# Performance work log

Measured on AMD Instinct MI355X. Metric: run time of the kernel, lower is better.

## Reference

```python
import jax, jax.numpy as jnp
import numpy as np

ALPHA = 1.702
LIMIT = 7.0


def setup_inputs() -> dict:
    key = jax.random.key(0)
    ks = jax.random.split(key, 6)
    T, H, D, E = 8192, 1024, 1024, 8
    hidden_states = jax.random.normal(ks[0], (T, H), dtype=jnp.float32)
    routing_weights = jax.random.uniform(ks[1], (T, E), dtype=jnp.float32)
    # 0.02 scale keeps activations in a sane range (original uses raw randn params)
    gate_up_proj = jax.random.normal(ks[2], (E, H, 2 * D), dtype=jnp.float32) * 0.02
    gate_up_proj_bias = jax.random.normal(ks[3], (E, 2 * D), dtype=jnp.float32) * 0.02
    down_proj = jax.random.normal(ks[4], (E, D, H), dtype=jnp.float32) * 0.02
    down_proj_bias = jax.random.normal(ks[5], (E, H), dtype=jnp.float32) * 0.02
    return {
        "hidden_states": hidden_states,
        "routing_weights": routing_weights,
        "gate_up_proj": gate_up_proj,
        "gate_up_proj_bias": gate_up_proj_bias,
        "down_proj": down_proj,
        "down_proj_bias": down_proj_bias,
    }


def reference(hidden_states, routing_weights, gate_up_proj, gate_up_proj_bias,
              down_proj, down_proj_bias):
    # hidden_states: [T, H]; routing_weights: [T, E] (batch_size == T in the torch code)
    B, H = hidden_states.shape[0], hidden_states.shape[-1]
    hs = hidden_states.reshape(-1, H)  # [T, H]
    # all-experts batched GEMM: [E, T, 2D]
    gate_up = jnp.einsum('th,ehd->etd', hs, gate_up_proj) + gate_up_proj_bias[:, None, :]
    gate = jnp.minimum(gate_up[..., ::2], LIMIT)          # [E, T, D]
    up = jnp.clip(gate_up[..., 1::2], -LIMIT, LIMIT)      # [E, T, D]
    glu = gate * jax.nn.sigmoid(gate * ALPHA)
    # down projection: [E, T, H]
    next_states = jnp.einsum('etd,edh->eth', (up + 1.0) * glu, down_proj) \
        + down_proj_bias[:, None, :]
    # routing-weighted combine over experts: [T, H]
    out = jnp.einsum('eth,te->th', next_states, routing_weights)
    return out.reshape(B, -1, H)  # [T, 1, H], matching final .view(batch_size, -1, hidden)
```

## Files before the change

kernel.cpp:

```cpp
#include <hip/hip_runtime.h>
#include <hip/hip_bf16.h>

#define T_DIM 8192
#define H_DIM 1024
#define D_DIM 1024
#define E_DIM 8
#define TWO_D 2048
#define K2 8192

#define ALPHA_C 1.702f
#define LIMIT_C 7.0f

typedef __attribute__((ext_vector_type(8))) short s8v;
typedef __attribute__((ext_vector_type(4))) float f4v;

__device__ __forceinline__ void g2l16(const void* g, void* l) {
    __builtin_amdgcn_global_load_lds((const __attribute__((address_space(1))) void*)g,
                                     (__attribute__((address_space(3))) void*)l, 16, 0, 0);
}

__device__ __forceinline__ unsigned short f2bf(float f) {
    __hip_bfloat16 h = __float2bfloat16(f);
    return __builtin_bit_cast(unsigned short, h);
}

#define FEN asm volatile("" ::: "memory")
#define BARR { FEN; __builtin_amdgcn_s_barrier(); FEN; }
#define VMW0 asm volatile("s_waitcnt vmcnt(0)" ::: "memory")


__global__ void f32_to_bf16_kernel(const float* __restrict__ in,
                                   unsigned short* __restrict__ out, size_t n) {
    size_t i = ((size_t)blockIdx.x * blockDim.x + threadIdx.x) * 4;
    if (i + 3 < n) {
        float4 v = *(const float4*)(in + i);
        ushort4 o;
        o.x = f2bf(v.x); o.y = f2bf(v.y); o.z = f2bf(v.z); o.w = f2bf(v.w);
        *(ushort4*)(out + i) = o;
    }
}

__global__ void transpose_conv_kernel(const float* __restrict__ in,
                                      unsigned short* __restrict__ out,
                                      int cols, size_t ibs, size_t obs, size_t ors,
                                      int remap) {
    __shared__ float t[32][33];
    const int b = blockIdx.z;
    const int c0 = blockIdx.x * 32, r0 = blockIdx.y * 32;
    const int tx = threadIdx.x & 31, ty = threadIdx.x >> 5;
    const float* ip = in + (size_t)b * ibs;
    #pragma unroll
    for (int i = 0; i < 4; ++i)
        t[ty + i * 8][tx] = ip[(size_t)(r0 + ty + i * 8) * cols + c0 + tx];
    __syncthreads();
    unsigned short* op = out + (size_t)b * obs;
    #pragma unroll
    for (int i = 0; i < 4; ++i) {
        int c = c0 + ty + i * 8;
        int nc = remap ? ((c & ~31) + ((c & 1) << 4) + ((c >> 1) & 15)) : c;
        op[(size_t)nc * ors + r0 + tx] = f2bf(t[tx][ty + i * 8]);
    }
}

__global__ void transpose_w3_tiled_kernel(const float* __restrict__ in,
                                          unsigned short* __restrict__ out) {
    __shared__ float t[32][33];
    const int e = blockIdx.z;
    const int c0 = blockIdx.x * 32;
    const int r0 = blockIdx.y * 32;
    const int tx = threadIdx.x & 31, ty = threadIdx.x >> 5;
    const float* ip = in + (size_t)e * D_DIM * H_DIM;
    #pragma unroll
    for (int i = 0; i < 4; ++i)
        t[ty + i * 8][tx] = ip[(size_t)(r0 + ty + i * 8) * H_DIM + c0 + tx];
    __syncthreads();
    #pragma unroll
    for (int i = 0; i < 4; ++i) {
        const int hcol = c0 + ty + i * 8;
        const int kk = e * D_DIM + r0 + tx;
        const int nt = hcol >> 7, rIn = hcol & 127;
        const int kt = kk >> 6, c = kk & 63;
        out[((size_t)nt * 128 + kt) * 8192 + rIn * 64 + (c ^ ((rIn & 7) << 3))] =
            f2bf(t[tx][ty + i * 8]);
    }
}


__global__ __launch_bounds__(256, 2) void gemm1_kernel(
    const short* __restrict__ Ag0,
    const short* __restrict__ Bg0,
    const float* __restrict__ b1,
    const float* __restrict__ rw,
    unsigned short* __restrict__ act2t)
{
    const int e = blockIdx.z;
    const int mBase = blockIdx.x * 128;
    const int nBase = blockIdx.y * 128;
    const int tid = threadIdx.x;
    const int lane = tid & 63;
    const int wave = tid >> 6;
    const int wm = wave >> 1, wn = wave & 1;
    const int cq = lane & 15, quad = lane >> 4;

    __shared__ __align__(16) short As[128 * 64];
    __shared__ __align__(16) short Bs[128 * 64];

    const short* Ag = Ag0 + (size_t)mBase * H_DIM;
    const short* Bg = Bg0 + ((size_t)e * TWO_D + nBase) * H_DIM;

    f4v acc[4][4];
    #pragma unroll
    for (int mt = 0; mt < 4; ++mt)
        #pragma unroll
        for (int nt = 0; nt < 4; ++nt)
            acc[mt][nt] = (f4v){0.f, 0.f, 0.f, 0.f};

    const int srow8 = lane >> 3;
    const int gco = ((lane & 7) ^ srow8) * 8;
    const int cq7 = cq & 7;

    for (int k0 = 0; k0 < H_DIM; k0 += 64) {
        #pragma unroll
        for (int i = 0; i < 4; ++i) {
            const int r = wave * 32 + i * 8 + srow8;
            g2l16(Ag + (size_t)r * H_DIM + k0 + gco, As + (wave * 32 + i * 8) * 64);
            g2l16(Bg + (size_t)r * H_DIM + k0 + gco, Bs + (wave * 32 + i * 8) * 64);
        }
        __syncthreads();
        #pragma unroll
        for (int h = 0; h < 2; ++h) {
            s8v af[4], bf[4];
            const int pc = (((h << 2) + quad) ^ cq7) * 8;
            #pragma unroll
            for (int i = 0; i < 4; ++i) {
                af[i] = *(const s8v*)(As + (wm * 64 + i * 16 + cq) * 64 + pc);
                bf[i] = *(const s8v*)(Bs + (wn * 64 + i * 16 + cq) * 64 + pc);
            }
            #pragma unroll
            for (int mt = 0; mt < 4; ++mt)
                #pragma unroll
                for (int nt = 0; nt < 4; ++nt)
                    acc[mt][nt] = __builtin_amdgcn_mfma_f32_16x16x32_bf16(
                        af[mt], bf[nt], acc[mt][nt], 0, 0, 0);
        }
        __syncthreads();
    }

    float rwv[4][4];
    #pragma unroll
    for (int mt = 0; mt < 4; ++mt)
        #pragma unroll
        for (int r = 0; r < 4; ++r)
            rwv[mt][r] = rw[(size_t)(mBase + wm * 64 + mt * 16 + quad * 4 + r) * E_DIM + e];

    const int kt_blk = e * 16 + (nBase >> 7);
    unsigned short* tb = act2t + ((size_t)blockIdx.x * 128 + kt_blk) * 8192;

    #pragma unroll
    for (int p = 0; p < 2; ++p) {
        const int j = (((nBase + wn * 64 + p * 32) >> 5) << 4) + cq;
        const float gb = b1[(size_t)e * TWO_D + 2 * j];
        const float ub = b1[(size_t)e * TWO_D + 2 * j + 1];
        const int c = wn * 32 + p * 16 + cq;
        #pragma unroll
        for (int mt = 0; mt < 4; ++mt) {
            #pragma unroll
            for (int r = 0; r < 4; ++r) {
                float gate = acc[mt][2 * p][r] + gb;
                float up   = acc[mt][2 * p + 1][r] + ub;
                gate = fminf(gate, LIMIT_C);
                up = fminf(fmaxf(up, -LIMIT_C), LIMIT_C);
                float glu = gate / (1.f + __expf(-ALPHA_C * gate));
                float a = (up + 1.f) * glu * rwv[mt][r];
                const int rIn = wm * 64 + mt * 16 + quad * 4 + r;
                tb[rIn * 64 + (c ^ ((rIn & 7) << 3))] = f2bf(a);
            }
        }
    }
}


__global__ __launch_bounds__(512, 1) void gemm2_kernel(
    const short* __restrict__ At,
    const short* __restrict__ Bt,
    const float* __restrict__ rw,
    const float* __restrict__ b3,
    float* __restrict__ out)
{
    const int id = blockIdx.x;
    const int mIdx = id & 31;
    const int nIdx = id >> 5;
    const int tid = threadIdx.x;
    const int lane = tid & 63;
    const int wave = tid >> 6;
    const int wm = wave >> 1, wn = wave & 1;
    const int cq = lane & 15, quad = lane >> 4;
    const int cq7 = cq & 7;

    __shared__ __align__(16) short As[2][256 * 64];
    __shared__ __align__(16) short Bs[2][128 * 64];

    f4v acc[4][4];
    #pragma unroll
    for (int mt = 0; mt < 4; ++mt)
        #pragma unroll
        for (int nt = 0; nt < 4; ++nt)
            acc[mt][nt] = (f4v){0.f, 0.f, 0.f, 0.f};

    const int lane8 = lane * 8;

#define G2STAGE(KT, BUF)                                                          \
    { const size_t _kt = (size_t)(KT);                                            \
      _Pragma("unroll")                                                           \
      for (int i = 0; i < 4; ++i) {                                               \
          const int R = wave * 32 + i * 8;                                        \
          const short* _s = At + ((size_t)(2 * mIdx + (R >> 7)) * 128 + _kt) * 8192 \
                          + (R & 127) * 64 + lane8;                               \
          g2l16(_s, &As[BUF][R * 64]);                                            \
      }                                                                           \
      _Pragma("unroll")                                                           \
      for (int i = 0; i < 2; ++i) {                                               \
          const int R = wave * 16 + i * 8;                                        \
          const short* _s = Bt + ((size_t)nIdx * 128 + _kt) * 8192 + R * 64 + lane8; \
          g2l16(_s, &Bs[BUF][R * 64]);                                            \
      } }

    G2STAGE(0, 0);
    VMW0;
    BARR;

    int cur = 0;
    #pragma unroll 1
    for (int kt = 0; kt < 128; ++kt) {
        if (kt + 1 < 128) { G2STAGE(kt + 1, cur ^ 1); }
        FEN;
        const short* Ab = As[cur];
        const short* Bb = Bs[cur];
        __builtin_amdgcn_s_setprio(1);
        #pragma unroll
        for (int h = 0; h < 2; ++h) {
            s8v af[4], bf[4];
            const int pc = (((h << 2) + quad) ^ cq7) * 8;
            #pragma unroll
            for (int i = 0; i < 4; ++i) {
                af[i] = *(const s8v*)(Ab + (wm * 64 + i * 16 + cq) * 64 + pc);
                bf[i] = *(const s8v*)(Bb + (wn * 64 + i * 16 + cq) * 64 + pc);
            }
            #pragma unroll
            for (int mt = 0; mt < 4; ++mt)
                #pragma unroll
                for (int nt = 0; nt < 4; ++nt)
                    acc[mt][nt] = __builtin_amdgcn_mfma_f32_16x16x32_bf16(
                        af[mt], bf[nt], acc[mt][nt], 0, 0, 0);
        }
        __builtin_amdgcn_s_setprio(0);
        VMW0;
        BARR;
        cur ^= 1;
    }

    const int mBase = mIdx * 256;
    const int nBase = nIdx * 128;
    #pragma unroll
    for (int mt = 0; mt < 4; ++mt) {
        #pragma unroll
        for (int r = 0; r < 4; ++r) {
            const int row = mBase + wm * 64 + mt * 16 + quad * 4 + r;
            const float4 rwa = *(const float4*)(rw + (size_t)row * E_DIM);
            const float4 rwb = *(const float4*)(rw + (size_t)row * E_DIM + 4);
            #pragma unroll
            for (int nt = 0; nt < 4; ++nt) {
                const int col = nBase + wn * 64 + nt * 16 + cq;
                float bias = rwa.x * b3[0 * H_DIM + col] + rwa.y * b3[1 * H_DIM + col]
                           + rwa.z * b3[2 * H_DIM + col] + rwa.w * b3[3 * H_DIM + col]
                           + rwb.x * b3[4 * H_DIM + col] + rwb.y * b3[5 * H_DIM + col]
                           + rwb.z * b3[6 * H_DIM + col] + rwb.w * b3[7 * H_DIM + col];
                out[(size_t)row * H_DIM + col] = acc[mt][nt][r] + bias;
            }
        }
    }
}


extern "C" void kernel_launch(void* const* d_in, const int* in_sizes, int n_in,
                              void* d_out, int out_size, void* d_ws, size_t ws_size,
                              hipStream_t stream) {
    const float* hs = (const float*)d_in[0];
    const float* rw = (const float*)d_in[1];
    const float* w1 = (const float*)d_in[2];
    const float* b1 = (const float*)d_in[3];
    const float* w3 = (const float*)d_in[4];
    const float* b3 = (const float*)d_in[5];
    float* out = (float*)d_out;

    char* ws = (char*)d_ws;
    unsigned short* hsb   = (unsigned short*)(ws);
    unsigned short* w1b   = (unsigned short*)(ws + ((size_t)16 << 20));
    unsigned short* w3t   = (unsigned short*)(ws + ((size_t)48 << 20));
    unsigned short* act2t = (unsigned short*)(ws + ((size_t)64 << 20));

    {
        size_t n = (size_t)T_DIM * H_DIM;
        f32_to_bf16_kernel<<<dim3(n / (256 * 4)), dim3(256), 0, stream>>>(hs, hsb, n);
    }
    transpose_conv_kernel<<<dim3(TWO_D / 32, H_DIM / 32, E_DIM), dim3(256), 0, stream>>>(
        w1, w1b, TWO_D, (size_t)H_DIM * TWO_D, (size_t)TWO_D * H_DIM, (size_t)H_DIM, 1);
    transpose_w3_tiled_kernel<<<dim3(H_DIM / 32, D_DIM / 32, E_DIM), dim3(256), 0, stream>>>(
        w3, w3t);
    gemm1_kernel<<<dim3(T_DIM / 128, TWO_D / 128, E_DIM), dim3(256), 0, stream>>>(
        (const short*)hsb, (const short*)w1b, b1, rw, act2t);
    gemm2_kernel<<<dim3(256), dim3(512), 0, stream>>>(
        (const short*)act2t, (const short*)w3t, rw, b3, out);
}
```

Baseline: 614.0 us.

## Split-K gemm2 into two halves, enlarge gemm1 tiles, move bias to reduce kernel

gemm2 now splits the 8192-long K dimension into two halves across 512 blocks of 256 threads, with each block computing a 256x128 tile. It drops the double-buffered LDS pipeline in favour of single-buffered loads. One half writes to out and the other to a workspace partial, and a new reduce kernel sums them and adds the routing-weighted down bias. gemm1's M tile doubles to 256 rows per block to reuse B fragments more. This is meant to raise occupancy and parallelism in gemm2, at the cost of an extra full-size fp32 read/write pass. The partial buffer reuses the hsb workspace region, which is safe only because gemm1 has already consumed hsb.

```diff
diff --git a/kernel.cpp b/kernel.cpp
--- a/kernel.cpp
+++ b/kernel.cpp
@@ -23,10 +23,6 @@
     __hip_bfloat16 h = __float2bfloat16(f);
     return __builtin_bit_cast(unsigned short, h);
 }
-
-#define FEN asm volatile("" ::: "memory")
-#define BARR { FEN; __builtin_amdgcn_s_barrier(); FEN; }
-#define VMW0 asm volatile("s_waitcnt vmcnt(0)" ::: "memory")
 
 
 __global__ void f32_to_bf16_kernel(const float* __restrict__ in,
@@ -85,6 +81,27 @@
     }
 }
 
+__global__ void reduce_bias_kernel(const float* __restrict__ p0f,
+                                   const float* __restrict__ rw,
+                                   const float* __restrict__ b3,
+                                   float* __restrict__ out) {
+    const int t = blockIdx.x;
+    const int h = threadIdx.x * 4;
+    const size_t idx = (size_t)t * H_DIM + h;
+    float r[E_DIM];
+    #pragma unroll
+    for (int e = 0; e < E_DIM; ++e) r[e] = rw[(size_t)t * E_DIM + e];
+    float4 v = *(const float4*)(out + idx);
+    float4 p = *(const float4*)(p0f + idx);
+    v.x += p.x; v.y += p.y; v.z += p.z; v.w += p.w;
+    #pragma unroll
+    for (int e = 0; e < E_DIM; ++e) {
+        float4 bb = *(const float4*)(b3 + (size_t)e * H_DIM + h);
+        v.x += r[e] * bb.x; v.y += r[e] * bb.y; v.z += r[e] * bb.z; v.w += r[e] * bb.w;
+    }
+    *(float4*)(out + idx) = v;
+}
+
 
 __global__ __launch_bounds__(256, 2) void gemm1_kernel(
     const short* __restrict__ Ag0,
@@ -94,188 +111,167 @@
     unsigned short* __restrict__ act2t)
 {
     const int e = blockIdx.z;
-    const int mBase = blockIdx.x * 128;
+    const int mBase = blockIdx.x * 256;
     const int nBase = blockIdx.y * 128;
     const int tid = threadIdx.x;
     const int lane = tid & 63;
     const int wave = tid >> 6;
     const int wm = wave >> 1, wn = wave & 1;
     const int cq = lane & 15, quad = lane >> 4;
-
-    __shared__ __align__(16) short As[128 * 64];
+    const int cq7 = cq & 7;
+
+    __shared__ __align__(16) short As[256 * 64];
     __shared__ __align__(16) short Bs[128 * 64];
 
     const short* Ag = Ag0 + (size_t)mBase * H_DIM;
     const short* Bg = Bg0 + ((size_t)e * TWO_D + nBase) * H_DIM;
 
-    f4v acc[4][4];
-    #pragma unroll
-    for (int mt = 0; mt < 4; ++mt)
+    f4v acc[8][4];
+    #pragma unroll
+    for (int mt = 0; mt < 8; ++mt)
         #pragma unroll
         for (int nt = 0; nt < 4; ++nt)
             acc[mt][nt] = (f4v){0.f, 0.f, 0.f, 0.f};
 
     const int srow8 = lane >> 3;
     const int gco = ((lane & 7) ^ srow8) * 8;
-    const int cq7 = cq & 7;
 
     for (int k0 = 0; k0 < H_DIM; k0 += 64) {
         #pragma unroll
+        for (int i = 0; i < 8; ++i) {
+            const int rb = i * 32 + wave * 8;
+            g2l16(Ag + (size_t)(rb + srow8) * H_DIM + k0 + gco, As + rb * 64);
+        }
+        #pragma unroll
         for (int i = 0; i < 4; ++i) {
-            const int r = wave * 32 + i * 8 + srow8;
-            g2l16(Ag + (size_t)r * H_DIM + k0 + gco, As + (wave * 32 + i * 8) * 64);
-            g2l16(Bg + (size_t)r * H_DIM + k0 + gco, Bs + (wave * 32 + i * 8) * 64);
+            const int rb = i * 32 + wave * 8;
+            g2l16(Bg + (size_t)(rb + srow8) * H_DIM + k0 + gco, Bs + rb * 64);
         }
         __syncthreads();
         #pragma unroll
         for (int h = 0; h < 2; ++h) {
-            s8v af[4], bf[4];
             const int pc = (((h << 2) + quad) ^ cq7) * 8;
-            #pragma unroll
-            for (int i = 0; i < 4; ++i) {
-                af[i] = *(const s8v*)(As + (wm * 64 + i * 16 + cq) * 64 + pc);
+            s8v bf[4];
+            #pragma unroll
+            for (int i = 0; i < 4; ++i)
                 bf[i] = *(const s8v*)(Bs + (wn * 64 + i * 16 + cq) * 64 + pc);
-            }
-            #pragma unroll
-            for (int mt = 0; mt < 4; ++mt)
+            #pragma unroll
+            for (int mt = 0; mt < 8; ++mt) {
+                const s8v af = *(const s8v*)(As + (wm * 128 + mt * 16 + cq) * 64 + pc);
                 #pragma unroll
                 for (int nt = 0; nt < 4; ++nt)
                     acc[mt][nt] = __builtin_amdgcn_mfma_f32_16x16x32_bf16(
-                        af[mt], bf[nt], acc[mt][nt], 0, 0, 0);
+                        af, bf[nt], acc[mt][nt], 0, 0, 0);
+            }
         }
         __syncthreads();
     }
 
-    float rwv[4][4];
-    #pragma unroll
-    for (int mt = 0; mt < 4; ++mt)
-        #pragma unroll
-        for (int r = 0; r < 4; ++r)
-            rwv[mt][r] = rw[(size_t)(mBase + wm * 64 + mt * 16 + quad * 4 + r) * E_DIM + e];
-
-    const int kt_blk = e * 16 + (nBase >> 7);
-    unsigned short* tb = act2t + ((size_t)blockIdx.x * 128 + kt_blk) * 8192;
-
+    const int kt = e * 16 + blockIdx.y;
     #pragma unroll
     for (int p = 0; p < 2; ++p) {
         const int j = (((nBase + wn * 64 + p * 32) >> 5) << 4) + cq;
         const float gb = b1[(size_t)e * TWO_D + 2 * j];
         const float ub = b1[(size_t)e * TWO_D + 2 * j + 1];
-        const int c = wn * 32 + p * 16 + cq;
-        #pragma unroll
-        for (int mt = 0; mt < 4; ++mt) {
+        const int c = (wn * 2 + p) * 16 + cq;
+        #pragma unroll
+        for (int mt = 0; mt < 8; ++mt) {
             #pragma unroll
             for (int r = 0; r < 4; ++r) {
+                const int rIn = wm * 128 + mt * 16 + quad * 4 + r;
+                const float rwv = rw[(size_t)(mBase + rIn) * E_DIM + e];
                 float gate = acc[mt][2 * p][r] + gb;
                 float up   = acc[mt][2 * p + 1][r] + ub;
                 gate = fminf(gate, LIMIT_C);
                 up = fminf(fmaxf(up, -LIMIT_C), LIMIT_C);
                 float glu = gate / (1.f + __expf(-ALPHA_C * gate));
-                float a = (up + 1.f) * glu * rwv[mt][r];
-                const int rIn = wm * 64 + mt * 16 + quad * 4 + r;
-                tb[rIn * 64 + (c ^ ((rIn & 7) << 3))] = f2bf(a);
+                float a = (up + 1.f) * glu * rwv;
+                unsigned short* tb = act2t +
+                    ((size_t)(blockIdx.x * 2 + (rIn >> 7)) * 128 + kt) * 8192;
+                const int row = rIn & 127;
+                tb[row * 64 + (c ^ ((row & 7) << 3))] = f2bf(a);
             }
         }
     }
 }
 
 
-__global__ __launch_bounds__(512, 1) void gemm2_kernel(
+__global__ __launch_bounds__(256, 2) void gemm2_kernel(
     const short* __restrict__ At,
     const short* __restrict__ Bt,
-    const float* __restrict__ rw,
-    const float* __restrict__ b3,
-    float* __restrict__ out)
+    float* __restrict__ out,
+    float* __restrict__ p0f)
 {
     const int id = blockIdx.x;
     const int mIdx = id & 31;
-    const int nIdx = id >> 5;
+    const int nIdx = (id >> 5) & 7;
+    const int ks = id >> 8;
     const int tid = threadIdx.x;
     const int lane = tid & 63;
     const int wave = tid >> 6;
     const int wm = wave >> 1, wn = wave & 1;
     const int cq = lane & 15, quad = lane >> 4;
     const int cq7 = cq & 7;
-
-    __shared__ __align__(16) short As[2][256 * 64];
-    __shared__ __align__(16) short Bs[2][128 * 64];
-
-    f4v acc[4][4];
-    #pragma unroll
-    for (int mt = 0; mt < 4; ++mt)
+    const int lane8 = lane * 8;
+
+    __shared__ __align__(16) short As[256 * 64];
+    __shared__ __align__(16) short Bs[128 * 64];
+
+    f4v acc[8][4];
+    #pragma unroll
+    for (int mt = 0; mt < 8; ++mt)
         #pragma unroll
         for (int nt = 0; nt < 4; ++nt)
             acc[mt][nt] = (f4v){0.f, 0.f, 0.f, 0.f};
 
-    const int lane8 = lane * 8;
-
-#define G2STAGE(KT, BUF)                                                          \
-    { const size_t _kt = (size_t)(KT);                                            \
-      _Pragma("unroll")                                                           \
-      for (int i = 0; i < 4; ++i) {                                               \
-          const int R = wave * 32 + i * 8;                                        \
-          const short* _s = At + ((size_t)(2 * mIdx + (R >> 7)) * 128 + _kt) * 8192 \
-                          + (R & 127) * 64 + lane8;                               \
-          g2l16(_s, &As[BUF][R * 64]);                                            \
-      }                                                                           \
-      _Pragma("unroll")                                                           \
-      for (int i = 0; i < 2; ++i) {                                               \
-          const int R = wave * 16 + i * 8;                                        \
-          const short* _s = Bt + ((size_t)nIdx * 128 + _kt) * 8192 + R * 64 + lane8; \
-          g2l16(_s, &Bs[BUF][R * 64]);                                            \
-      } }
-
-    G2STAGE(0, 0);
-    VMW0;
-    BARR;
-
-    int cur = 0;
     #pragma unroll 1
-    for (int kt = 0; kt < 128; ++kt) {
-        if (kt + 1 < 128) { G2STAGE(kt + 1, cur ^ 1); }
-        FEN;
-        const short* Ab = As[cur];
-        const short* Bb = Bs[cur];
-        __builtin_amdgcn_s_setprio(1);
+    for (int s = 0; s < 64; ++s) {
+        const int kt = ks * 64 + s;
+        #pragma unroll
+        for (int i = 0; i < 8; ++i) {
+            const int R = i * 32 + wave * 8;
+            const short* src = At +
+                ((size_t)(2 * mIdx + (R >> 7)) * 128 + kt) * 8192 + (R & 127) * 64 + lane8;
+            g2l16(src, As + R * 64);
+        }
+        #pragma unroll
+        for (int i = 0; i < 4; ++i) {
+            const int R = i * 32 + wave * 8;
+            const short* src = Bt + ((size_t)nIdx * 128 + kt) * 8192 + R * 64 + lane8;
+            g2l16(src, Bs + R * 64);
+        }
+        __syncthreads();
         #pragma unroll
         for (int h = 0; h < 2; ++h) {
-            s8v af[4], bf[4];
             const int pc = (((h << 2) + quad) ^ cq7) * 8;
-            #pragma unroll
-            for (int i = 0; i < 4; ++i) {
-                af[i] = *(const s8v*)(Ab + (wm * 64 + i * 16 + cq) * 64 + pc);
-                bf[i] = *(const s8v*)(Bb + (wn * 64 + i * 16 + cq) * 64 + pc);
-            }
-            #pragma unroll
-            for (int mt = 0; mt < 4; ++mt)
+            s8v bf[4];
+            #pragma unroll
+            for (int i = 0; i < 4; ++i)
+                bf[i] = *(const s8v*)(Bs + (wn * 64 + i * 16 + cq) * 64 + pc);
+            #pragma unroll
+            for (int mt = 0; mt < 8; ++mt) {
+                const s8v af = *(const s8v*)(As + (wm * 128 + mt * 16 + cq) * 64 + pc);
                 #pragma unroll
                 for (int nt = 0; nt < 4; ++nt)
                     acc[mt][nt] = __builtin_amdgcn_mfma_f32_16x16x32_bf16(
-                        af[mt], bf[nt], acc[mt][nt], 0, 0, 0);
-        }
-        __builtin_amdgcn_s_setprio(0);
-        VMW0;
-        BARR;
-        cur ^= 1;
-    }
-
+                        af, bf[nt], acc[mt][nt], 0, 0, 0);
+            }
+        }
+        __syncthreads();
+    }
+
+    float* dst = (ks == 0) ? out : p0f;
     const int mBase = mIdx * 256;
     const int nBase = nIdx * 128;
     #pragma unroll
-    for (int mt = 0; mt < 4; ++mt) {
+    for (int mt = 0; mt < 8; ++mt) {
         #pragma unroll
         for (int r = 0; r < 4; ++r) {
-            const int row = mBase + wm * 64 + mt * 16 + quad * 4 + r;
-            const float4 rwa = *(const float4*)(rw + (size_t)row * E_DIM);
-            const float4 rwb = *(const float4*)(rw + (size_t)row * E_DIM + 4);
+            const int row = mBase + wm * 128 + mt * 16 + quad * 4 + r;
             #pragma unroll
             for (int nt = 0; nt < 4; ++nt) {
                 const int col = nBase + wn * 64 + nt * 16 + cq;
-                float bias = rwa.x * b3[0 * H_DIM + col] + rwa.y * b3[1 * H_DIM + col]
-                           + rwa.z * b3[2 * H_DIM + col] + rwa.w * b3[3 * H_DIM + col]
-                           + rwb.x * b3[4 * H_DIM + col] + rwb.y * b3[5 * H_DIM + col]
-                           + rwb.z * b3[6 * H_DIM + col] + rwb.w * b3[7 * H_DIM + col];
-                out[(size_t)row * H_DIM + col] = acc[mt][nt][r] + bias;
+                dst[(size_t)row * H_DIM + col] = acc[mt][nt][r];
             }
         }
     }
@@ -298,6 +294,7 @@
     unsigned short* w1b   = (unsigned short*)(ws + ((size_t)16 << 20));
     unsigned short* w3t   = (unsigned short*)(ws + ((size_t)48 << 20));
     unsigned short* act2t = (unsigned short*)(ws + ((size_t)64 << 20));
+    float* p0f = (float*)(ws);
 
     {
         size_t n = (size_t)T_DIM * H_DIM;
@@ -307,8 +304,10 @@
         w1, w1b, TWO_D, (size_t)H_DIM * TWO_D, (size_t)TWO_D * H_DIM, (size_t)H_DIM, 1);
     transpose_w3_tiled_kernel<<<dim3(H_DIM / 32, D_DIM / 32, E_DIM), dim3(256), 0, stream>>>(
         w3, w3t);
-    gemm1_kernel<<<dim3(T_DIM / 128, TWO_D / 128, E_DIM), dim3(256), 0, stream>>>(
+    gemm1_kernel<<<dim3(T_DIM / 256, TWO_D / 128, E_DIM), dim3(256), 0, stream>>>(
         (const short*)hsb, (const short*)w1b, b1, rw, act2t);
-    gemm2_kernel<<<dim3(256), dim3(512), 0, stream>>>(
-        (const short*)act2t, (const short*)w3t, rw, b3, out);
-}
+    gemm2_kernel<<<dim3(512), dim3(256), 0, stream>>>(
+        (const short*)act2t, (const short*)w3t, out, p0f);
+    reduce_bias_kernel<<<dim3(T_DIM), dim3(H_DIM / 4), 0, stream>>>(
+        p0f, rw, b3, out);
+}
```

Result: faster. 581.5 us (-5.3%).
